# Optimization experiments

Hardware: AMD Instinct MI355X
Metric: run time of the kernel (lower is better)

## Reference

```python
import jax, jax.numpy as jnp
import numpy as np

B, LQ, LK = 4, 256, 512
DQ, DK, DV = 512, 512, 512
H = 256
NEG = -1e6


def setup_inputs() -> dict:
    key = jax.random.key(0)
    ks = jax.random.split(key, 7)
    queries = jax.random.normal(ks[0], (B, LQ, DQ), dtype=jnp.float32)
    keys = jax.random.normal(ks[1], (B, LK, DK), dtype=jnp.float32)
    values = jax.random.normal(ks[2], (B, LK, DV), dtype=jnp.float32)
    valid_lens = jax.random.randint(ks[3], (B,), 1, LK + 1).astype(jnp.int32)
    # learned params (Linear without bias): store as (in, out) so x @ W matches torch x @ W.T
    Wq = jax.random.normal(ks[4], (DQ, H), dtype=jnp.float32) * (1.0 / np.sqrt(DQ))
    Wk = jax.random.normal(ks[5], (DK, H), dtype=jnp.float32) * (1.0 / np.sqrt(DK))
    wv = jax.random.normal(ks[6], (H,), dtype=jnp.float32) * (1.0 / np.sqrt(H))
    return {"queries": queries, "keys": keys, "values": values,
            "valid_lens": valid_lens, "Wq": Wq, "Wk": Wk, "wv": wv}


def reference(queries, keys, values, valid_lens, Wq, Wk, wv):
    q = jnp.einsum('bqd,dh->bqh', queries, Wq)          # (B,Lq,H)
    k = jnp.einsum('bkd,dh->bkh', keys, Wk)             # (B,Lk,H)
    feats = jnp.tanh(q[:, :, None, :] + k[:, None, :, :])  # (B,Lq,Lk,H)
    scores = jnp.einsum('bqkh,h->bqk', feats, wv)        # (B,Lq,Lk)
    mask = jnp.arange(LK)[None, None, :] < valid_lens[:, None, None]  # (B,1,Lk)
    attn = jax.nn.softmax(jnp.where(mask, scores, NEG), axis=-1)
    return jnp.einsum('bqk,bkv->bqv', attn, values)      # (B,Lq,Dv)
```

## Files before the change

kernel.cpp:

```cpp
#include <hip/hip_runtime.h>

#define B_   4
#define LQ_  256
#define LK_  512
#define DIN_ 512
#define H_   256
#define DV_  512

#define L2E 1.4426950408889634f

__global__ __launch_bounds__(256) void proj_partial_kernel(
    const float* __restrict__ Q, const float* __restrict__ K,
    const float* __restrict__ Wq, const float* __restrict__ Wk,
    const int* __restrict__ valid_lens,
    float* __restrict__ qpart, float* __restrict__ ekTpart) {
  __shared__ float xs[64][68];
  __shared__ float ws[64][132];

  const int blk = blockIdx.x;
  const bool isQ = blk < 128;
  int b, row0, h0, ds;
  if (isQ) {
    ds = blk & 3; h0 = ((blk >> 2) & 1) * 128;
    const int rt = blk >> 3;
    b = rt >> 2; row0 = (rt & 3) * 64;
  } else {
    const int u = blk - 128;
    ds = u & 7; h0 = ((u >> 3) & 1) * 128;
    const int rt = u >> 4;
    b = rt & 3; row0 = (rt >> 2) * 64;
    if (row0 >= valid_lens[b]) return;
  }
  const int L = isQ ? LQ_ : LK_;
  const int dspan = isQ ? 128 : 64;
  const float* __restrict__ X  = (isQ ? Q : K) + ((size_t)(b * L + row0)) * DIN_ + ds * dspan;
  const float* __restrict__ Wb = (isQ ? Wq : Wk) + (size_t)(ds * dspan) * H_ + h0;

  const int t = threadIdx.x;
  const int hthr = t & 31;
  const int rthr = t >> 5;

  float acc[8][4];
#pragma unroll
  for (int r = 0; r < 8; ++r)
#pragma unroll
    for (int c = 0; c < 4; ++c) acc[r][c] = 0.f;

  for (int dd = 0; dd < dspan; dd += 64) {
    __syncthreads();
#pragma unroll
    for (int u = 0; u < 4; ++u) {
      const int f = t + 256 * u;
      const int r = f >> 4, c4 = (f & 15) << 2;
      *(float4*)&xs[r][c4] = *(const float4*)&X[(size_t)r * DIN_ + dd + c4];
    }
#pragma unroll
    for (int u = 0; u < 8; ++u) {
      const int f = t + 256 * u;
      const int k = f >> 5, c4 = (f & 31) << 2;
      *(float4*)&ws[k][c4] = *(const float4*)&Wb[(size_t)(dd + k) * H_ + c4];
    }
    __syncthreads();

    for (int k = 0; k < 64; k += 8) {
      float4 w4[8];
#pragma unroll
      for (int k8 = 0; k8 < 8; ++k8)
        w4[k8] = *(const float4*)&ws[k + k8][4 * hthr];
#pragma unroll
      for (int rr = 0; rr < 8; ++rr) {
        const float4 xa = *(const float4*)&xs[rthr * 8 + rr][k];
        const float4 xb = *(const float4*)&xs[rthr * 8 + rr][k + 4];
        const float xv[8] = {xa.x, xa.y, xa.z, xa.w, xb.x, xb.y, xb.z, xb.w};
#pragma unroll
        for (int k8 = 0; k8 < 8; ++k8) {
          acc[rr][0] = fmaf(xv[k8], w4[k8].x, acc[rr][0]);
          acc[rr][1] = fmaf(xv[k8], w4[k8].y, acc[rr][1]);
          acc[rr][2] = fmaf(xv[k8], w4[k8].z, acc[rr][2]);
          acc[rr][3] = fmaf(xv[k8], w4[k8].w, acc[rr][3]);
        }
      }
    }
  }

  if (isQ) {
    float* dst = qpart + (size_t)ds * (B_ * LQ_ * H_);
#pragma unroll
    for (int rr = 0; rr < 8; ++rr) {
      const int row = row0 + rthr * 8 + rr;
      float4 o = {acc[rr][0], acc[rr][1], acc[rr][2], acc[rr][3]};
      *(float4*)&dst[(size_t)(b * LQ_ + row) * H_ + h0 + 4 * hthr] = o;
    }
  } else {
    float* dst = ekTpart + (size_t)ds * (B_ * H_ * LK_);
#pragma unroll
    for (int c = 0; c < 4; ++c) {
      const int h = h0 + 4 * hthr + c;
      float* p = &dst[((size_t)b * H_ + h) * LK_ + row0 + rthr * 8];
      float4 lo = {acc[0][c], acc[1][c], acc[2][c], acc[3][c]};
      float4 hi = {acc[4][c], acc[5][c], acc[6][c], acc[7][c]};
      *(float4*)p = lo;
      *(float4*)(p + 4) = hi;
    }
  }
}

__global__ __launch_bounds__(512) void combine_ek_kernel(
    const float* __restrict__ ekTpart, float* __restrict__ ek2) {
  const int k4 = blockIdx.x * 512 + threadIdx.x;
  const size_t KN4 = (size_t)B_ * H_ * LK_ / 4;
  const float4* src = (const float4*)ekTpart;
  float4 s = src[k4];
#pragma unroll
  for (int p = 1; p < 8; ++p) {
    const float4 v = src[p * KN4 + k4];
    s.x += v.x; s.y += v.y; s.z += v.z; s.w += v.w;
  }
  float4 o;
  o.x = exp2f(fminf(fmaxf(s.x * (2.f * L2E), -126.f), 126.f));
  o.y = exp2f(fminf(fmaxf(s.y * (2.f * L2E), -126.f), 126.f));
  o.z = exp2f(fminf(fmaxf(s.z * (2.f * L2E), -126.f), 126.f));
  o.w = exp2f(fminf(fmaxf(s.w * (2.f * L2E), -126.f), 126.f));
  ((float4*)ek2)[k4] = o;
}

__global__ __launch_bounds__(512) void fused_attn_kernel(
    const float* __restrict__ qpart, const float* __restrict__ ek2,
    const float* __restrict__ wv, const int* __restrict__ valid_lens,
    const float* __restrict__ V, float* __restrict__ out) {
  __shared__ float eqs[2][260];
  __shared__ float wvs[256];
  __shared__ float2 p2s[LK_];
  __shared__ float redm[8][2], reds[8][2];
  __shared__ float wsum_s;

  const int blk = blockIdx.x;
  const int b  = (blk & 3) ^ ((blk >> 8) & 1);
  const int i0 = (blk >> 2) * 2;
  const int vl = valid_lens[b];
  const int t = threadIdx.x;
  const int lane = t & 63, wave = t >> 6;

  const size_t QN = (size_t)B_ * LQ_ * H_;
  {
    const int i = t >> 8, h = t & 255;
    const size_t base = (size_t)(b * LQ_ + i0 + i) * H_ + h;
    const float v = qpart[base] + qpart[QN + base] +
                    qpart[2 * QN + base] + qpart[3 * QN + base];
    eqs[i][h] = exp2f(fminf(fmaxf(v * (2.f * L2E), -126.f), 126.f));
  }
  if (t < 256) wvs[t] = wv[t];
  if (t < 64) {
    float s = wv[t] + wv[t + 64] + wv[t + 128] + wv[t + 192];
#pragma unroll
    for (int off = 32; off; off >>= 1) s += __shfl_xor(s, off);
    if (t == 0) wsum_s = s;
  }
  __syncthreads();
  const float Wsum = wsum_s;

  const bool valid = t < vl;
  float s[2] = {-3.0e38f, -3.0e38f};
  if (valid) {
    const float* __restrict__ kb = ek2 + (size_t)b * H_ * LK_ + t;
    float a0 = 0.f, a1 = 0.f;
    for (int h = 0; h < H_; h += 8) {
      float kv[8];
#pragma unroll
      for (int u = 0; u < 8; ++u)
        kv[u] = kb[(size_t)(h + u) * LK_];
      const float4 wa = *(const float4*)&wvs[h];
      const float4 wb = *(const float4*)&wvs[h + 4];
      const float ww[8] = {wa.x, wa.y, wa.z, wa.w, wb.x, wb.y, wb.z, wb.w};
      const float4 q0a = *(const float4*)&eqs[0][h];
      const float4 q0b = *(const float4*)&eqs[0][h + 4];
      const float4 q1a = *(const float4*)&eqs[1][h];
      const float4 q1b = *(const float4*)&eqs[1][h + 4];
      const float q0[8] = {q0a.x, q0a.y, q0a.z, q0a.w, q0b.x, q0b.y, q0b.z, q0b.w};
      const float q1[8] = {q1a.x, q1a.y, q1a.z, q1a.w, q1b.x, q1b.y, q1b.z, q1b.w};
#pragma unroll
      for (int u = 0; u < 8; ++u) {
        a0 = fmaf(ww[u], __builtin_amdgcn_rcpf(fmaf(q0[u], kv[u], 1.f)), a0);
        a1 = fmaf(ww[u], __builtin_amdgcn_rcpf(fmaf(q1[u], kv[u], 1.f)), a1);
      }
    }
    s[0] = fmaf(-2.f, a0, Wsum);
    s[1] = fmaf(-2.f, a1, Wsum);
  }

  float m[2] = {s[0], s[1]};
#pragma unroll
  for (int off = 32; off; off >>= 1)
#pragma unroll
    for (int i = 0; i < 2; ++i) m[i] = fmaxf(m[i], __shfl_xor(m[i], off));
  if (lane == 0)
#pragma unroll
    for (int i = 0; i < 2; ++i) redm[wave][i] = m[i];
  __syncthreads();
  float e[2], sum[2];
#pragma unroll
  for (int i = 0; i < 2; ++i) {
    float mx = redm[0][i];
#pragma unroll
    for (int w = 1; w < 8; ++w) mx = fmaxf(mx, redm[w][i]);
    e[i] = valid ? __expf(s[i] - mx) : 0.f;
    sum[i] = e[i];
  }
#pragma unroll
  for (int off = 32; off; off >>= 1)
#pragma unroll
    for (int i = 0; i < 2; ++i) sum[i] += __shfl_xor(sum[i], off);
  if (lane == 0)
#pragma unroll
    for (int i = 0; i < 2; ++i) reds[wave][i] = sum[i];
  __syncthreads();
  {
    float tot[2];
#pragma unroll
    for (int i = 0; i < 2; ++i) {
      tot[i] = reds[0][i];
#pragma unroll
      for (int w = 1; w < 8; ++w) tot[i] += reds[w][i];
    }
    float2 pv;
    pv.x = e[0] * __builtin_amdgcn_rcpf(tot[0]);
    pv.y = e[1] * __builtin_amdgcn_rcpf(tot[1]);
    p2s[t] = pv;
  }
  __syncthreads();

  const float* __restrict__ Vb = V + (size_t)b * LK_ * DV_ + t;
  float a0 = 0.f, a1 = 0.f;
  int j = 0;
  const int jv = vl & ~7;
  for (; j < jv; j += 8) {
    float v[8];
#pragma unroll
    for (int u = 0; u < 8; ++u) v[u] = Vb[(size_t)(j + u) * DV_];
#pragma unroll
    for (int u = 0; u < 8; ++u) {
      const float2 pp = p2s[j + u];
      a0 = fmaf(pp.x, v[u], a0);
      a1 = fmaf(pp.y, v[u], a1);
    }
  }
  for (; j < vl; ++j) {
    const float v = Vb[(size_t)j * DV_];
    const float2 pp = p2s[j];
    a0 = fmaf(pp.x, v, a0);
    a1 = fmaf(pp.y, v, a1);
  }
  out[(size_t)(b * LQ_ + i0) * DV_ + t]     = a0;
  out[(size_t)(b * LQ_ + i0 + 1) * DV_ + t] = a1;
}

extern "C" void kernel_launch(void* const* d_in, const int* in_sizes, int n_in,
                              void* d_out, int out_size, void* d_ws, size_t ws_size,
                              hipStream_t stream) {
  const float* queries    = (const float*)d_in[0];
  const float* keys       = (const float*)d_in[1];
  const float* values     = (const float*)d_in[2];
  const int*   valid_lens = (const int*)d_in[3];
  const float* Wq         = (const float*)d_in[4];
  const float* Wk         = (const float*)d_in[5];
  const float* wv         = (const float*)d_in[6];
  float* out = (float*)d_out;

  char* ws = (char*)d_ws;
  float* qpart   = (float*)ws;
  float* ekTpart = (float*)(ws + (size_t)( 4 << 20));
  float* ek2     = (float*)(ws + (size_t)(20 << 20));

  proj_partial_kernel<<<640, 256, 0, stream>>>(
      queries, keys, Wq, Wk, valid_lens, qpart, ekTpart);
  combine_ek_kernel<<<256, 512, 0, stream>>>(ekTpart, ek2);
  fused_attn_kernel<<<512, 512, 0, stream>>>(
      qpart, ek2, wv, valid_lens, values, out);
}
```

Baseline: 52.47 us.

## Split H reduction across thread halves for short valid lengths and drop max pass

When the batch's valid length is at most 256, the two halves of the block each compute half of the H reduction for the same key column and combine the partial sums through shared memory. Otherwise half the threads would sit idle. The softmax max-reduction is removed: since |scores| are bounded by the sum of |wv|, exp is computed directly without subtracting the maximum. This saves one reduction and one barrier but relies on the scores staying small enough to avoid overflow. The inner loop also loads 16 keys per step instead of 8.

```diff
diff --git a/kernel.cpp b/kernel.cpp
--- a/kernel.cpp
+++ b/kernel.cpp
@@ -130,8 +130,9 @@
     const float* __restrict__ V, float* __restrict__ out) {
   __shared__ float eqs[2][260];
   __shared__ float wvs[256];
+  __shared__ float ph[2][2][260];
   __shared__ float2 p2s[LK_];
-  __shared__ float redm[8][2], reds[8][2];
+  __shared__ float reds[8][2];
   __shared__ float wsum_s;
 
   const int blk = blockIdx.x;
@@ -161,49 +162,76 @@
 
   const bool valid = t < vl;
   float s[2] = {-3.0e38f, -3.0e38f};
-  if (valid) {
-    const float* __restrict__ kb = ek2 + (size_t)b * H_ * LK_ + t;
-    float a0 = 0.f, a1 = 0.f;
-    for (int h = 0; h < H_; h += 8) {
-      float kv[8];
-#pragma unroll
-      for (int u = 0; u < 8; ++u)
-        kv[u] = kb[(size_t)(h + u) * LK_];
-      const float4 wa = *(const float4*)&wvs[h];
-      const float4 wb = *(const float4*)&wvs[h + 4];
-      const float ww[8] = {wa.x, wa.y, wa.z, wa.w, wb.x, wb.y, wb.z, wb.w};
-      const float4 q0a = *(const float4*)&eqs[0][h];
-      const float4 q0b = *(const float4*)&eqs[0][h + 4];
-      const float4 q1a = *(const float4*)&eqs[1][h];
-      const float4 q1b = *(const float4*)&eqs[1][h + 4];
-      const float q0[8] = {q0a.x, q0a.y, q0a.z, q0a.w, q0b.x, q0b.y, q0b.z, q0b.w};
-      const float q1[8] = {q1a.x, q1a.y, q1a.z, q1a.w, q1b.x, q1b.y, q1b.z, q1b.w};
-#pragma unroll
-      for (int u = 0; u < 8; ++u) {
-        a0 = fmaf(ww[u], __builtin_amdgcn_rcpf(fmaf(q0[u], kv[u], 1.f)), a0);
-        a1 = fmaf(ww[u], __builtin_amdgcn_rcpf(fmaf(q1[u], kv[u], 1.f)), a1);
+  if (vl > 256) {
+    if (valid) {
+      const float* __restrict__ kb = ek2 + (size_t)b * H_ * LK_ + t;
+      float a0 = 0.f, a1 = 0.f;
+      for (int h = 0; h < H_; h += 16) {
+        float kv[16];
+#pragma unroll
+        for (int u = 0; u < 16; ++u)
+          kv[u] = kb[(size_t)(h + u) * LK_];
+#pragma unroll
+        for (int g = 0; g < 4; ++g) {
+          const float4 w4  = *(const float4*)&wvs[h + 4 * g];
+          const float4 q0v = *(const float4*)&eqs[0][h + 4 * g];
+          const float4 q1v = *(const float4*)&eqs[1][h + 4 * g];
+          const float ww[4] = {w4.x, w4.y, w4.z, w4.w};
+          const float q0[4] = {q0v.x, q0v.y, q0v.z, q0v.w};
+          const float q1[4] = {q1v.x, q1v.y, q1v.z, q1v.w};
+#pragma unroll
+          for (int u = 0; u < 4; ++u) {
+            const float k2 = kv[4 * g + u];
+            a0 = fmaf(ww[u], __builtin_amdgcn_rcpf(fmaf(q0[u], k2, 1.f)), a0);
+            a1 = fmaf(ww[u], __builtin_amdgcn_rcpf(fmaf(q1[u], k2, 1.f)), a1);
+          }
+        }
       }
-    }
-    s[0] = fmaf(-2.f, a0, Wsum);
-    s[1] = fmaf(-2.f, a1, Wsum);
-  }
-
-  float m[2] = {s[0], s[1]};
-#pragma unroll
-  for (int off = 32; off; off >>= 1)
-#pragma unroll
-    for (int i = 0; i < 2; ++i) m[i] = fmaxf(m[i], __shfl_xor(m[i], off));
-  if (lane == 0)
-#pragma unroll
-    for (int i = 0; i < 2; ++i) redm[wave][i] = m[i];
-  __syncthreads();
+      s[0] = fmaf(-2.f, a0, Wsum);
+      s[1] = fmaf(-2.f, a1, Wsum);
+    }
+  } else {
+    const int j = t & 255;
+    const int hb = (t >> 8) * 128;
+    if (j < vl) {
+      const float* __restrict__ kb = ek2 + (size_t)b * H_ * LK_ + j;
+      float a0 = 0.f, a1 = 0.f;
+      for (int hh = 0; hh < 128; hh += 16) {
+        const int h = hb + hh;
+        float kv[16];
+#pragma unroll
+        for (int u = 0; u < 16; ++u)
+          kv[u] = kb[(size_t)(h + u) * LK_];
+#pragma unroll
+        for (int g = 0; g < 4; ++g) {
+          const float4 w4  = *(const float4*)&wvs[h + 4 * g];
+          const float4 q0v = *(const float4*)&eqs[0][h + 4 * g];
+          const float4 q1v = *(const float4*)&eqs[1][h + 4 * g];
+          const float ww[4] = {w4.x, w4.y, w4.z, w4.w};
+          const float q0[4] = {q0v.x, q0v.y, q0v.z, q0v.w};
+          const float q1[4] = {q1v.x, q1v.y, q1v.z, q1v.w};
+#pragma unroll
+          for (int u = 0; u < 4; ++u) {
+            const float k2 = kv[4 * g + u];
+            a0 = fmaf(ww[u], __builtin_amdgcn_rcpf(fmaf(q0[u], k2, 1.f)), a0);
+            a1 = fmaf(ww[u], __builtin_amdgcn_rcpf(fmaf(q1[u], k2, 1.f)), a1);
+          }
+        }
+      }
+      ph[t >> 8][0][j] = a0;
+      ph[t >> 8][1][j] = a1;
+    }
+    __syncthreads();
+    if (valid) {
+      s[0] = fmaf(-2.f, ph[0][0][t] + ph[1][0][t], Wsum);
+      s[1] = fmaf(-2.f, ph[0][1][t] + ph[1][1][t], Wsum);
+    }
+  }
+
   float e[2], sum[2];
 #pragma unroll
   for (int i = 0; i < 2; ++i) {
-    float mx = redm[0][i];
-#pragma unroll
-    for (int w = 1; w < 8; ++w) mx = fmaxf(mx, redm[w][i]);
-    e[i] = valid ? __expf(s[i] - mx) : 0.f;
+    e[i] = valid ? exp2f(s[i] * L2E) : 0.f;
     sum[i] = e[i];
   }
 #pragma unroll
```

Result: no change. 51.98 us (-0.9%).

## Split fused attention into score/exp and AV kernels with fp16 values

Applied to the files above, without the earlier changes.

The fused attention kernel is split into two kernels. A scores kernel spreads the key dimension over four chunks per query pair, skips chunks past valid_len, writes unnormalized exp scores and per-chunk partial sums. An AV kernel then normalizes and multiplies by a half-precision copy of V that the combine kernel produces, and the combine kernel also precomputes the wv sum. The aim is more parallelism in the tanh/score phase and less V bandwidth. In exchange it adds a kernel launch and an intermediate global buffer, and the softmax no longer subtracts the max, which risks overflow and fp16 precision loss.

```diff
diff --git a/kernel.cpp b/kernel.cpp
--- a/kernel.cpp
+++ b/kernel.cpp
@@ -1,4 +1,5 @@
 #include <hip/hip_runtime.h>
+#include <hip/hip_fp16.h>
 
 #define B_   4
 #define LQ_  256
@@ -105,153 +106,154 @@
   }
 }
 
-__global__ __launch_bounds__(512) void combine_ek_kernel(
-    const float* __restrict__ ekTpart, float* __restrict__ ek2) {
-  const int k4 = blockIdx.x * 512 + threadIdx.x;
-  const size_t KN4 = (size_t)B_ * H_ * LK_ / 4;
-  const float4* src = (const float4*)ekTpart;
-  float4 s = src[k4];
-#pragma unroll
-  for (int p = 1; p < 8; ++p) {
-    const float4 v = src[p * KN4 + k4];
-    s.x += v.x; s.y += v.y; s.z += v.z; s.w += v.w;
-  }
-  float4 o;
-  o.x = exp2f(fminf(fmaxf(s.x * (2.f * L2E), -126.f), 126.f));
-  o.y = exp2f(fminf(fmaxf(s.y * (2.f * L2E), -126.f), 126.f));
-  o.z = exp2f(fminf(fmaxf(s.z * (2.f * L2E), -126.f), 126.f));
-  o.w = exp2f(fminf(fmaxf(s.w * (2.f * L2E), -126.f), 126.f));
-  ((float4*)ek2)[k4] = o;
-}
-
-__global__ __launch_bounds__(512) void fused_attn_kernel(
+__global__ __launch_bounds__(512) void combine_kernel(
+    const float* __restrict__ ekTpart, const float* __restrict__ V,
+    const float* __restrict__ wv,
+    float* __restrict__ ek2, __half* __restrict__ Vh, float* __restrict__ wsum) {
+  const int blk = blockIdx.x;
+  const int t = threadIdx.x;
+  if (blk < 256) {
+    const int k4 = blk * 512 + t;
+    const size_t KN4 = (size_t)B_ * H_ * LK_ / 4;
+    const float4* src = (const float4*)ekTpart;
+    float4 s = src[k4];
+#pragma unroll
+    for (int p = 1; p < 8; ++p) {
+      const float4 v = src[p * KN4 + k4];
+      s.x += v.x; s.y += v.y; s.z += v.z; s.w += v.w;
+    }
+    float4 o;
+    o.x = exp2f(fminf(fmaxf(s.x * (2.f * L2E), -126.f), 126.f));
+    o.y = exp2f(fminf(fmaxf(s.y * (2.f * L2E), -126.f), 126.f));
+    o.z = exp2f(fminf(fmaxf(s.z * (2.f * L2E), -126.f), 126.f));
+    o.w = exp2f(fminf(fmaxf(s.w * (2.f * L2E), -126.f), 126.f));
+    ((float4*)ek2)[k4] = o;
+    if (blk == 0 && t < 64) {
+      float sw = wv[t] + wv[t + 64] + wv[t + 128] + wv[t + 192];
+#pragma unroll
+      for (int off = 32; off; off >>= 1) sw += __shfl_xor(sw, off);
+      if (t == 0) *wsum = sw;
+    }
+  } else {
+    const int q4 = (blk - 256) * 512 + t;
+    const float4 v = ((const float4*)V)[q4];
+    ((__half2*)Vh)[2 * q4]     = __floats2half2_rn(v.x, v.y);
+    ((__half2*)Vh)[2 * q4 + 1] = __floats2half2_rn(v.z, v.w);
+  }
+}
+
+__global__ __launch_bounds__(256) void scores_exp_kernel(
     const float* __restrict__ qpart, const float* __restrict__ ek2,
-    const float* __restrict__ wv, const int* __restrict__ valid_lens,
-    const float* __restrict__ V, float* __restrict__ out) {
+    const float* __restrict__ wv, const float* __restrict__ wsum,
+    const int* __restrict__ valid_lens,
+    float* __restrict__ e_out, float* __restrict__ sums) {
   __shared__ float eqs[2][260];
   __shared__ float wvs[256];
-  __shared__ float2 p2s[LK_];
-  __shared__ float redm[8][2], reds[8][2];
-  __shared__ float wsum_s;
-
-  const int blk = blockIdx.x;
-  const int b  = (blk & 3) ^ ((blk >> 8) & 1);
-  const int i0 = (blk >> 2) * 2;
+  __shared__ float red[4];
+
+  const int blk = blockIdx.x;
+  const int b  = blk & 3;
+  const int c  = (blk >> 2) & 3;
+  const int ip = blk >> 4;
+  const int i0 = ip * 2;
   const int vl = valid_lens[b];
-  const int t = threadIdx.x;
-  const int lane = t & 63, wave = t >> 6;
+  const int j0 = c * 128;
+  if (j0 >= vl) return;
+  const int t = threadIdx.x;
+  const int jj = t & 127, row = t >> 7;
 
   const size_t QN = (size_t)B_ * LQ_ * H_;
-  {
-    const int i = t >> 8, h = t & 255;
+#pragma unroll
+  for (int u = 0; u < 2; ++u) {
+    const int idx = t + 256 * u;
+    const int i = idx >> 8, h = idx & 255;
     const size_t base = (size_t)(b * LQ_ + i0 + i) * H_ + h;
     const float v = qpart[base] + qpart[QN + base] +
                     qpart[2 * QN + base] + qpart[3 * QN + base];
     eqs[i][h] = exp2f(fminf(fmaxf(v * (2.f * L2E), -126.f), 126.f));
   }
-  if (t < 256) wvs[t] = wv[t];
-  if (t < 64) {
-    float s = wv[t] + wv[t + 64] + wv[t + 128] + wv[t + 192];
-#pragma unroll
-    for (int off = 32; off; off >>= 1) s += __shfl_xor(s, off);
-    if (t == 0) wsum_s = s;
-  }
+  wvs[t] = wv[t];
   __syncthreads();
-  const float Wsum = wsum_s;
-
-  const bool valid = t < vl;
-  float s[2] = {-3.0e38f, -3.0e38f};
-  if (valid) {
-    const float* __restrict__ kb = ek2 + (size_t)b * H_ * LK_ + t;
-    float a0 = 0.f, a1 = 0.f;
-    for (int h = 0; h < H_; h += 8) {
-      float kv[8];
-#pragma unroll
-      for (int u = 0; u < 8; ++u)
+  const float Wsum = *wsum;
+
+  const int j = j0 + jj;
+  float eexp = 0.f;
+  if (j < vl) {
+    const float* __restrict__ kb = ek2 + (size_t)b * H_ * LK_ + j;
+    float a = 0.f;
+    for (int h = 0; h < H_; h += 16) {
+      float kv[16];
+#pragma unroll
+      for (int u = 0; u < 16; ++u)
         kv[u] = kb[(size_t)(h + u) * LK_];
-      const float4 wa = *(const float4*)&wvs[h];
-      const float4 wb = *(const float4*)&wvs[h + 4];
-      const float ww[8] = {wa.x, wa.y, wa.z, wa.w, wb.x, wb.y, wb.z, wb.w};
-      const float4 q0a = *(const float4*)&eqs[0][h];
-      const float4 q0b = *(const float4*)&eqs[0][h + 4];
-      const float4 q1a = *(const float4*)&eqs[1][h];
-      const float4 q1b = *(const float4*)&eqs[1][h + 4];
-      const float q0[8] = {q0a.x, q0a.y, q0a.z, q0a.w, q0b.x, q0b.y, q0b.z, q0b.w};
-      const float q1[8] = {q1a.x, q1a.y, q1a.z, q1a.w, q1b.x, q1b.y, q1b.z, q1b.w};
-#pragma unroll
-      for (int u = 0; u < 8; ++u) {
-        a0 = fmaf(ww[u], __builtin_amdgcn_rcpf(fmaf(q0[u], kv[u], 1.f)), a0);
-        a1 = fmaf(ww[u], __builtin_amdgcn_rcpf(fmaf(q1[u], kv[u], 1.f)), a1);
+#pragma unroll
+      for (int g = 0; g < 4; ++g) {
+        const float4 w4 = *(const float4*)&wvs[h + 4 * g];
+        const float4 q4 = *(const float4*)&eqs[row][h + 4 * g];
+        const float ww[4] = {w4.x, w4.y, w4.z, w4.w};
+        const float qq[4] = {q4.x, q4.y, q4.z, q4.w};
+#pragma unroll
+        for (int u = 0; u < 4; ++u)
+          a = fmaf(ww[u], __builtin_amdgcn_rcpf(fmaf(qq[u], kv[4 * g + u], 1.f)), a);
       }
     }
-    s[0] = fmaf(-2.f, a0, Wsum);
-    s[1] = fmaf(-2.f, a1, Wsum);
-  }
-
-  float m[2] = {s[0], s[1]};
-#pragma unroll
-  for (int off = 32; off; off >>= 1)
-#pragma unroll
-    for (int i = 0; i < 2; ++i) m[i] = fmaxf(m[i], __shfl_xor(m[i], off));
-  if (lane == 0)
-#pragma unroll
-    for (int i = 0; i < 2; ++i) redm[wave][i] = m[i];
+    const float score = fmaf(-2.f, a, Wsum);
+    eexp = exp2f(score * L2E);
+    e_out[(size_t)(b * LQ_ + i0 + row) * LK_ + j] = eexp;
+  }
+  float s = eexp;
+#pragma unroll
+  for (int off = 32; off; off >>= 1) s += __shfl_xor(s, off);
+  if ((t & 63) == 0) red[t >> 6] = s;
   __syncthreads();
-  float e[2], sum[2];
-#pragma unroll
-  for (int i = 0; i < 2; ++i) {
-    float mx = redm[0][i];
-#pragma unroll
-    for (int w = 1; w < 8; ++w) mx = fmaxf(mx, redm[w][i]);
-    e[i] = valid ? __expf(s[i] - mx) : 0.f;
-    sum[i] = e[i];
-  }
-#pragma unroll
-  for (int off = 32; off; off >>= 1)
-#pragma unroll
-    for (int i = 0; i < 2; ++i) sum[i] += __shfl_xor(sum[i], off);
-  if (lane == 0)
-#pragma unroll
-    for (int i = 0; i < 2; ++i) reds[wave][i] = sum[i];
-  __syncthreads();
-  {
-    float tot[2];
-#pragma unroll
-    for (int i = 0; i < 2; ++i) {
-      tot[i] = reds[0][i];
-#pragma unroll
-      for (int w = 1; w < 8; ++w) tot[i] += reds[w][i];
-    }
-    float2 pv;
-    pv.x = e[0] * __builtin_amdgcn_rcpf(tot[0]);
-    pv.y = e[1] * __builtin_amdgcn_rcpf(tot[1]);
-    p2s[t] = pv;
-  }
-  __syncthreads();
-
-  const float* __restrict__ Vb = V + (size_t)b * LK_ * DV_ + t;
+  if (t == 0)   sums[(size_t)(b * LQ_ + i0) * 4 + c]     = red[0] + red[1];
+  if (t == 128) sums[(size_t)(b * LQ_ + i0 + 1) * 4 + c] = red[2] + red[3];
+}
+
+__global__ __launch_bounds__(512) void av_kernel(
+    const float* __restrict__ e_in, const float* __restrict__ sums,
+    const __half* __restrict__ Vh, const int* __restrict__ valid_lens,
+    float* __restrict__ out) {
+  const int blk = blockIdx.x;
+  const int b  = (blk & 3) ^ ((blk >> 8) & 1);
+  const int i0 = (blk >> 2) * 2;
+  const int vl = valid_lens[b];
+  const int t = threadIdx.x;
+
+  const int nc = min(4, (vl + 127) >> 7);
+  float tot0 = 0.f, tot1 = 0.f;
+  for (int c = 0; c < nc; ++c) {
+    tot0 += sums[(size_t)(b * LQ_ + i0) * 4 + c];
+    tot1 += sums[(size_t)(b * LQ_ + i0 + 1) * 4 + c];
+  }
+  const float inv0 = __builtin_amdgcn_rcpf(tot0);
+  const float inv1 = __builtin_amdgcn_rcpf(tot1);
+
+  const float* __restrict__ e0 = e_in + (size_t)(b * LQ_ + i0) * LK_;
+  const float* __restrict__ e1 = e0 + LK_;
+  const __half* __restrict__ Vb = Vh + (size_t)b * LK_ * DV_ + t;
+
   float a0 = 0.f, a1 = 0.f;
   int j = 0;
   const int jv = vl & ~7;
   for (; j < jv; j += 8) {
     float v[8];
 #pragma unroll
-    for (int u = 0; u < 8; ++u) v[u] = Vb[(size_t)(j + u) * DV_];
+    for (int u = 0; u < 8; ++u)
+      v[u] = __half2float(Vb[(size_t)(j + u) * DV_]);
 #pragma unroll
     for (int u = 0; u < 8; ++u) {
-      const float2 pp = p2s[j + u];
-      a0 = fmaf(pp.x, v[u], a0);
-      a1 = fmaf(pp.y, v[u], a1);
+      a0 = fmaf(e0[j + u], v[u], a0);
+      a1 = fmaf(e1[j + u], v[u], a1);
     }
   }
   for (; j < vl; ++j) {
-    const float v = Vb[(size_t)j * DV_];
-    const float2 pp = p2s[j];
-    a0 = fmaf(pp.x, v, a0);
-    a1 = fmaf(pp.y, v, a1);
-  }
-  out[(size_t)(b * LQ_ + i0) * DV_ + t]     = a0;
-  out[(size_t)(b * LQ_ + i0 + 1) * DV_ + t] = a1;
+    const float v = __half2float(Vb[(size_t)j * DV_]);
+    a0 = fmaf(e0[j], v, a0);
+    a1 = fmaf(e1[j], v, a1);
+  }
+  out[(size_t)(b * LQ_ + i0) * DV_ + t]     = a0 * inv0;
+  out[(size_t)(b * LQ_ + i0 + 1) * DV_ + t] = a1 * inv1;
 }
 
 extern "C" void kernel_launch(void* const* d_in, const int* in_sizes, int n_in,
@@ -267,13 +269,20 @@
   float* out = (float*)d_out;
 
   char* ws = (char*)d_ws;
-  float* qpart   = (float*)ws;
-  float* ekTpart = (float*)(ws + (size_t)( 4 << 20));
-  float* ek2     = (float*)(ws + (size_t)(20 << 20));
+  float*  qpart   = (float*)ws;
+  float*  ekTpart = (float*)(ws + (size_t)( 4 << 20));
+  float*  ek2     = (float*)(ws + (size_t)(20 << 20));
+  float*  e_buf   = (float*)(ws + (size_t)(22 << 20));
+  __half* Vh      = (__half*)(ws + (size_t)(24 << 20));
+  float*  sums    = (float*)(ws + (size_t)(26 << 20));
+  float*  wsum    = (float*)(ws + (size_t)(26 << 20) + 16384);
 
   proj_partial_kernel<<<640, 256, 0, stream>>>(
       queries, keys, Wq, Wk, valid_lens, qpart, ekTpart);
-  combine_ek_kernel<<<256, 512, 0, stream>>>(ekTpart, ek2);
-  fused_attn_kernel<<<512, 512, 0, stream>>>(
-      qpart, ek2, wv, valid_lens, values, out);
-}
+  combine_kernel<<<768, 512, 0, stream>>>(
+      ekTpart, values, wv, ek2, Vh, wsum);
+  scores_exp_kernel<<<2048, 256, 0, stream>>>(
+      qpart, ek2, wv, wsum, valid_lens, e_buf, sums);
+  av_kernel<<<512, 512, 0, stream>>>(
+      e_buf, sums, Vh, valid_lens, out);
+}
```

Result: slower. 64.42 us (+22.8%).
